# Kernel optimization log

Measured on AMD Instinct MI355X. Metric: run time of the kernel, lower is better.

Reference implementation:

```python
import jax, jax.numpy as jnp
import numpy as np

B, S, D, H = 4, 1024, 1024, 16
DK = D // H  # 64; concat head dim is 2*DK


def setup_inputs() -> dict:
    key = jax.random.key(0)
    ks = jax.random.split(key, 32)
    inp = {}
    for i, name in enumerate(["query_g", "key_g", "query_a", "key_a", "value_a"]):
        inp[name] = jax.random.normal(ks[i], (B, S, D), dtype=jnp.float32)
    inp["mask"] = jnp.ones((B, S, S), dtype=jnp.int32)
    w_scale = 1.0 / np.sqrt(D).astype(np.float32)
    # torch Linear weights are [out, in]; y = x @ W.T + b
    param_shapes = [
        ("Wqg", (D, D)), ("bqg", (D,)), ("Wkg", (D, D)), ("bkg", (D,)),
        ("Wqa", (D, D)), ("bqa", (D,)), ("Wka", (D, D)), ("bka", (D,)),
        ("Wva", (D, D)), ("bva", (D,)),
        ("Wgate", (D, 2 * D)), ("bgate", (D,)),
        ("Winfo", (D, D)), ("binfo", (D,)),
    ]
    for j, (name, shape) in enumerate(param_shapes):
        inp[name] = jax.random.normal(ks[5 + j], shape, dtype=jnp.float32) * w_scale
    return inp


def reference(query_g, key_g, query_a, key_a, value_a, mask,
              Wqg, bqg, Wkg, bkg, Wqa, bqa, Wka, bka, Wva, bva,
              Wgate, bgate, Winfo, binfo):
    def heads(x, W, b):
        # [B,S,D] -> [B,H,S,DK]
        return (x @ W.T + b).reshape(B, S, H, DK).transpose(0, 2, 1, 3)

    qg = heads(query_g, Wqg, bqg)
    kg = heads(key_g, Wkg, bkg)
    qa = heads(query_a, Wqa, bqa)
    ka = heads(key_a, Wka, bka)
    va = heads(value_a, Wva, bva)

    q = jnp.concatenate([qa, qg], axis=-1)  # [B,H,S,2*DK]
    k = jnp.concatenate([ka, kg], axis=-1)
    scores = jnp.einsum('bhqd,bhkd->bhqk', q, k) / np.float32(np.sqrt(2 * DK))
    scores = jnp.where(mask[:, None, :, :] == 0, jnp.float32(-1e9), scores)
    p_attn = jax.nn.softmax(scores, axis=-1)  # dropout is identity in eval
    x = jnp.einsum('bhqk,bhkd->bhqd', p_attn, va)
    x = x.transpose(0, 2, 1, 3).reshape(B, S, D)

    # GLU branch (dropout_glu is identity in eval); linears_out is identity
    gate = jax.nn.sigmoid(jnp.concatenate([query_a, query_g], axis=-1) @ Wgate.T + bgate)
    info = x @ Winfo.T + binfo
    return gate * info
```

## Files before the change

kernel.cpp:

```cpp
#include <hip/hip_runtime.h>


typedef unsigned short u16;
typedef __bf16 bf16x8 __attribute__((ext_vector_type(8)));
typedef float f32x4 __attribute__((ext_vector_type(4)));

#define DEV static __device__ __forceinline__

DEV u16 f2bf(float x) {
  union { __bf16 h; u16 u; } c;
  c.h = (__bf16)x;
  return c.u;
}
DEV float bf2f(u16 h) { return __uint_as_float(((unsigned)h) << 16); }

DEV bf16x8 cvt8(float4 a, float4 b) {
  bf16x8 v;
  v[0] = (__bf16)a.x; v[1] = (__bf16)a.y; v[2] = (__bf16)a.z; v[3] = (__bf16)a.w;
  v[4] = (__bf16)b.x; v[5] = (__bf16)b.y; v[6] = (__bf16)b.z; v[7] = (__bf16)b.w;
  return v;
}

struct Args {
  const float* act[5];
  const float* W[7];
  const float* bias[7];
  u16 *q_buf, *k_buf, *va_t, *x_buf, *g_buf;
  float* out;
};

__global__ __launch_bounds__(256, 2) void gemm_kernel(Args P, int unit_override) {
  __shared__ __align__(16) u16 As[128 * 40];
  __shared__ __align__(16) u16 Bs[128 * 40];

  int unit, bid;
  if (unit_override >= 0) { unit = unit_override; bid = blockIdx.x; }
  else { unit = blockIdx.x >> 8; bid = blockIdx.x & 255; }
  const int bm = bid & 31;
  const int bn = bid >> 5;

  const int tid = threadIdx.x;
  const int lane = tid & 63;
  const int wid = tid >> 6;
  const int wq = wid >> 1, wn = wid & 1;
  const int cl = lane & 15;
  const int gl = lane >> 4;

  const float *A0, *A1 = nullptr, *Wp, *bp;
  int nkt, mode;
  switch (unit) {
    case 0: A0 = P.act[0]; A1 = P.act[1]; Wp = P.W[5]; bp = P.bias[5]; nkt = 64; mode = 0; break;
    case 1: A0 = P.act[0]; Wp = P.W[0]; bp = P.bias[0]; nkt = 32; mode = 1; break;
    case 2: A0 = P.act[1]; Wp = P.W[1]; bp = P.bias[1]; nkt = 32; mode = 2; break;
    case 3: A0 = P.act[2]; Wp = P.W[2]; bp = P.bias[2]; nkt = 32; mode = 3; break;
    case 4: A0 = P.act[3]; Wp = P.W[3]; bp = P.bias[3]; nkt = 32; mode = 4; break;
    case 5: A0 = P.act[4]; Wp = P.W[4]; bp = P.bias[4]; nkt = 32; mode = 5; break;
    default: A0 = nullptr; Wp = P.W[6]; bp = P.bias[6]; nkt = 32; mode = 6; break;
  }
  const int K = nkt * 32;

  f32x4 acc[4][4];
  const f32x4 vzero = {0.f, 0.f, 0.f, 0.f};
#pragma unroll
  for (int i = 0; i < 4; i++)
#pragma unroll
    for (int j = 0; j < 4; j++) acc[i][j] = vzero;

  int arow[2], apn[2];
#pragma unroll
  for (int j = 0; j < 2; j++) {
    int f = (wid * 2 + j) * 64 + lane;
    arow[j] = f >> 2;
    apn[j] = f & 3;
  }

  float4 ra[2][2], rb[2][2];
  bf16x8 ra6[2];

  auto stage = [&](int kt) {
    const float* Abase;
    int akoff;
    if (A1 && kt >= 32) { Abase = A1; akoff = (kt - 32) * 32; }
    else { Abase = A0; akoff = kt * 32; }
#pragma unroll
    for (int j = 0; j < 2; j++) {
      size_t ae = (size_t)(bm * 128 + arow[j]) * 1024 + akoff + apn[j] * 8;
      size_t we = (size_t)(bn * 128 + arow[j]) * K + kt * 32 + apn[j] * 8;
      if (mode == 6) {
        ra6[j] = *(const bf16x8*)(const void*)(P.x_buf + ae);
      } else {
        const float* p = Abase + ae;
        ra[j][0] = *(const float4*)(const void*)p;
        ra[j][1] = *(const float4*)(const void*)(p + 4);
      }
      const float* q = Wp + we;
      rb[j][0] = *(const float4*)(const void*)q;
      rb[j][1] = *(const float4*)(const void*)(q + 4);
    }
  };

  stage(0);

  for (int kt = 0; kt < nkt; kt++) {
    __syncthreads();
#pragma unroll
    for (int j = 0; j < 2; j++) {
      *(bf16x8*)(void*)&As[arow[j] * 40 + apn[j] * 8] =
          (mode == 6) ? ra6[j] : cvt8(ra[j][0], ra[j][1]);
      *(bf16x8*)(void*)&Bs[arow[j] * 40 + apn[j] * 8] = cvt8(rb[j][0], rb[j][1]);
    }
    __syncthreads();

    bf16x8 af[4], bfr[4];
#pragma unroll
    for (int mi = 0; mi < 4; mi++)
      af[mi] = *(const bf16x8*)(const void*)&As[(wq * 64 + mi * 16 + cl) * 40 + gl * 8];
#pragma unroll
    for (int nj = 0; nj < 4; nj++)
      bfr[nj] = *(const bf16x8*)(const void*)&Bs[(wn * 64 + nj * 16 + cl) * 40 + gl * 8];

    if (kt + 1 < nkt) stage(kt + 1);

#pragma unroll
    for (int mi = 0; mi < 4; mi++)
#pragma unroll
      for (int nj = 0; nj < 4; nj++)
        acc[mi][nj] = __builtin_amdgcn_mfma_f32_16x16x32_bf16(af[mi], bfr[nj], acc[mi][nj], 0, 0, 0);
  }

  const int rowbase = bm * 128 + wq * 64;
  const int colbase = bn * 128 + wn * 64;
#pragma unroll
  for (int mi = 0; mi < 4; mi++) {
#pragma unroll
    for (int nj = 0; nj < 4; nj++) {
      const int gn = colbase + nj * 16 + cl;
      const float bias = bp[gn];
      const int gm0 = rowbase + mi * 16 + gl * 4;
      if (mode == 0) {
#pragma unroll
        for (int r = 0; r < 4; r++) {
          float v = acc[mi][nj][r] + bias;
          float s = 1.0f / (1.0f + __expf(-v));
          size_t idx = (size_t)(gm0 + r) * 1024 + gn;
          if (P.g_buf) P.g_buf[idx] = f2bf(s);
          else P.out[idx] = s;
        }
      } else if (mode <= 4) {
        u16* dst = (mode <= 2) ? P.q_buf : P.k_buf;
        const int part = (mode == 2 || mode == 4) ? 1 : 0;
        const int h = gn >> 6, dk = gn & 63;
#pragma unroll
        for (int r = 0; r < 4; r++) {
          int gm = gm0 + r;
          int b = gm >> 10, s = gm & 1023;
          dst[(((size_t)(b * 16 + h)) * 1024 + s) * 128 + part * 64 + dk] =
              f2bf(acc[mi][nj][r] + bias);
        }
      } else if (mode == 5) {
        const int h = gn >> 6, dk = gn & 63;
        int b = gm0 >> 10, s = gm0 & 1023;
        ushort4 pk;
        pk.x = f2bf(acc[mi][nj][0] + bias);
        pk.y = f2bf(acc[mi][nj][1] + bias);
        pk.z = f2bf(acc[mi][nj][2] + bias);
        pk.w = f2bf(acc[mi][nj][3] + bias);
        *(ushort4*)&P.va_t[(((size_t)(b * 16 + h)) * 64 + dk) * 1024 + s] = pk;
      } else {
#pragma unroll
        for (int r = 0; r < 4; r++) {
          size_t idx = (size_t)(gm0 + r) * 1024 + gn;
          float g = P.g_buf ? bf2f(P.g_buf[idx]) : P.out[idx];
          P.out[idx] = (acc[mi][nj][r] + bias) * g;
        }
      }
    }
  }
}

__global__ __launch_bounds__(256, 2) void attn_kernel(const u16* __restrict__ q_buf,
                                                      const u16* __restrict__ k_buf,
                                                      const u16* __restrict__ va_t,
                                                      const int* __restrict__ mask,
                                                      u16* __restrict__ x_buf) {
  __shared__ __align__(16) u16 Ks[64 * 136];
  __shared__ __align__(16) u16 Vs[64 * 72];
  __shared__ __align__(16) u16 Ps[4 * 32 * 72];
  __shared__ int mflags[16];

  const int tid = threadIdx.x;
  const int lane = tid & 63;
  const int wid = tid >> 6;
  const int cl = lane & 15;
  const int gl = lane >> 4;

  const int qt = blockIdx.x & 7;
  const int bh = blockIdx.x >> 3;
  const int b = bh >> 4, h = bh & 15;
  const u16* qh = q_buf + (size_t)bh * 1024 * 128;
  const u16* kh = k_buf + (size_t)bh * 1024 * 128;
  const u16* vh = va_t + (size_t)bh * 64 * 1024;
  const int s0 = qt * 128;

  if (tid < 16) mflags[tid] = 1;
  __syncthreads();
  {
    const int* mbase = mask + ((size_t)b * 1024 + s0) * 1024 + tid * 4;
    int ok = 1;
#pragma unroll 4
    for (int i = 0; i < 128; i++) {
      const int4 m4 = *(const int4*)(const void*)(mbase + (size_t)i * 1024);
      if (!(m4.x && m4.y && m4.z && m4.w)) ok = 0;
    }
    if (!ok) atomicAnd(&mflags[tid >> 4], 0);
  }
  __syncthreads();

  bf16x8 aq[2][4];
#pragma unroll
  for (int mi = 0; mi < 2; mi++) {
    int row = s0 + wid * 32 + mi * 16 + cl;
#pragma unroll
    for (int kk = 0; kk < 4; kk++)
      aq[mi][kk] = *(const bf16x8*)(const void*)&qh[(size_t)row * 128 + kk * 32 + gl * 8];
  }

  f32x4 acc_o[2][4];
  float l_part[2][4];
  const f32x4 vzero = {0.f, 0.f, 0.f, 0.f};
#pragma unroll
  for (int mi = 0; mi < 2; mi++) {
#pragma unroll
    for (int nj = 0; nj < 4; nj++) acc_o[mi][nj] = vzero;
#pragma unroll
    for (int r = 0; r < 4; r++) l_part[mi][r] = 0.f;
  }

  const float scale = 0.08838834764831845f;
  u16* pw = &Ps[wid * 32 * 72];

  int krow[4], kp[4], vrow[2], vp[2];
#pragma unroll
  for (int j = 0; j < 4; j++) {
    int f = (wid * 4 + j) * 64 + lane;
    krow[j] = f >> 4; kp[j] = f & 15;
  }
#pragma unroll
  for (int j = 0; j < 2; j++) {
    int f = (wid * 2 + j) * 64 + lane;
    vrow[j] = f >> 3; vp[j] = f & 7;
  }

  bf16x8 kv[4], vv[2];
  auto stageKV = [&](int kt) {
#pragma unroll
    for (int j = 0; j < 4; j++)
      kv[j] = *(const bf16x8*)(const void*)&kh[(size_t)(kt * 64 + krow[j]) * 128 + kp[j] * 8];
#pragma unroll
    for (int j = 0; j < 2; j++)
      vv[j] = *(const bf16x8*)(const void*)&vh[(size_t)vrow[j] * 1024 + kt * 64 + vp[j] * 8];
  };

  stageKV(0);

  for (int kt = 0; kt < 16; kt++) {
    __syncthreads();
#pragma unroll
    for (int j = 0; j < 4; j++)
      *(bf16x8*)(void*)&Ks[krow[j] * 136 + kp[j] * 8] = kv[j];
#pragma unroll
    for (int j = 0; j < 2; j++)
      *(bf16x8*)(void*)&Vs[vrow[j] * 72 + vp[j] * 8] = vv[j];
    __syncthreads();

    if (kt < 15) stageKV(kt + 1);

    f32x4 sc[2][4];
#pragma unroll
    for (int mi = 0; mi < 2; mi++)
#pragma unroll
      for (int nj = 0; nj < 4; nj++) sc[mi][nj] = vzero;
#pragma unroll
    for (int kk = 0; kk < 4; kk++) {
      bf16x8 bk[4];
#pragma unroll
      for (int nj = 0; nj < 4; nj++)
        bk[nj] = *(const bf16x8*)(const void*)&Ks[(nj * 16 + cl) * 136 + (kk * 4 + gl) * 8];
#pragma unroll
      for (int mi = 0; mi < 2; mi++)
#pragma unroll
        for (int nj = 0; nj < 4; nj++)
          sc[mi][nj] = __builtin_amdgcn_mfma_f32_16x16x32_bf16(aq[mi][kk], bk[nj], sc[mi][nj], 0, 0, 0);
    }

    const bool fastm = (mflags[kt] != 0);
#pragma unroll
    for (int mi = 0; mi < 2; mi++) {
#pragma unroll
      for (int nj = 0; nj < 4; nj++) {
        int key = kt * 64 + nj * 16 + cl;
#pragma unroll
        for (int r = 0; r < 4; r++) {
          int lrow = mi * 16 + gl * 4 + r;
          float sv = fminf(sc[mi][nj][r] * scale, 30.0f);
          float pv;
          if (fastm) {
            pv = __expf(sv);
          } else {
            int qrow = s0 + wid * 32 + lrow;
            int mv = mask[((size_t)b * 1024 + qrow) * 1024 + key];
            pv = (mv != 0) ? __expf(sv) : 0.0f;
          }
          l_part[mi][r] += pv;
          pw[lrow * 72 + nj * 16 + cl] = f2bf(pv);
        }
      }
    }

#pragma unroll
    for (int kk = 0; kk < 2; kk++) {
      bf16x8 ap[2], bv[4];
#pragma unroll
      for (int mi = 0; mi < 2; mi++)
        ap[mi] = *(const bf16x8*)(const void*)&pw[(mi * 16 + cl) * 72 + kk * 32 + gl * 8];
#pragma unroll
      for (int nj = 0; nj < 4; nj++)
        bv[nj] = *(const bf16x8*)(const void*)&Vs[(nj * 16 + cl) * 72 + (kk * 4 + gl) * 8];
#pragma unroll
      for (int mi = 0; mi < 2; mi++)
#pragma unroll
        for (int nj = 0; nj < 4; nj++)
          acc_o[mi][nj] = __builtin_amdgcn_mfma_f32_16x16x32_bf16(ap[mi], bv[nj], acc_o[mi][nj], 0, 0, 0);
    }
  }

#pragma unroll
  for (int mi = 0; mi < 2; mi++)
#pragma unroll
    for (int r = 0; r < 4; r++) {
      float s = l_part[mi][r];
      s += __shfl_xor(s, 1);
      s += __shfl_xor(s, 2);
      s += __shfl_xor(s, 4);
      s += __shfl_xor(s, 8);
      l_part[mi][r] = 1.0f / s;
    }

#pragma unroll
  for (int mi = 0; mi < 2; mi++)
#pragma unroll
    for (int nj = 0; nj < 4; nj++)
#pragma unroll
      for (int r = 0; r < 4; r++) {
        int srow = s0 + wid * 32 + mi * 16 + gl * 4 + r;
        int dv = nj * 16 + cl;
        float v = acc_o[mi][nj][r] * l_part[mi][r];
        x_buf[((size_t)b * 1024 + srow) * 1024 + h * 64 + dv] = f2bf(v);
      }
}

extern "C" void kernel_launch(void* const* d_in, const int* in_sizes, int n_in,
                              void* d_out, int out_size, void* d_ws, size_t ws_size,
                              hipStream_t stream) {
  (void)in_sizes; (void)n_in; (void)out_size;
  const int* mask = (const int*)d_in[5];

  char* ws = (char*)d_ws;
  u16* q_buf = (u16*)(ws);
  u16* k_buf = (u16*)(ws + ((size_t)16 << 20));
  u16* va_t  = (u16*)(ws + ((size_t)32 << 20));
  u16* x_buf = (u16*)(ws + ((size_t)40 << 20));
  u16* g_buf = (ws_size >= ((size_t)56 << 20)) ? (u16*)(ws + ((size_t)48 << 20)) : nullptr;

  Args P;
  P.act[0] = (const float*)d_in[2];
  P.act[1] = (const float*)d_in[0];
  P.act[2] = (const float*)d_in[3];
  P.act[3] = (const float*)d_in[1];
  P.act[4] = (const float*)d_in[4];
  P.W[0] = (const float*)d_in[10];  P.bias[0] = (const float*)d_in[11];
  P.W[1] = (const float*)d_in[6];   P.bias[1] = (const float*)d_in[7];
  P.W[2] = (const float*)d_in[12];  P.bias[2] = (const float*)d_in[13];
  P.W[3] = (const float*)d_in[8];   P.bias[3] = (const float*)d_in[9];
  P.W[4] = (const float*)d_in[14];  P.bias[4] = (const float*)d_in[15];
  P.W[5] = (const float*)d_in[16];  P.bias[5] = (const float*)d_in[17];
  P.W[6] = (const float*)d_in[18];  P.bias[6] = (const float*)d_in[19];
  P.q_buf = q_buf; P.k_buf = k_buf; P.va_t = va_t; P.x_buf = x_buf;
  P.g_buf = g_buf; P.out = (float*)d_out;

  hipLaunchKernelGGL(gemm_kernel, dim3(1536), dim3(256), 0, stream, P, -1);
  hipLaunchKernelGGL(attn_kernel, dim3(512), dim3(256), 0, stream,
                     q_buf, k_buf, va_t, mask, x_buf);
  hipLaunchKernelGGL(gemm_kernel, dim3(256), dim3(256), 0, stream, P, 6);
}
```

Before: 430.0 us.

## Pre-convert inputs to bf16 and use double-buffered global-to-LDS DMA GEMM

Adds a conversion kernel that casts all activations and weights from fp32 to bf16 into workspace once per call. A new GEMM kernel then streams bf16 tiles straight into LDS with global_load_lds, double-buffered, at higher occupancy. The aim is to halve the bytes the GEMMs read and to drop the per-tile in-register conversion and LDS store work. In exchange it adds an extra memory-bound pass plus a launch, and it only runs when the workspace is at least 112 MB; otherwise the old path is kept.

Measured after the change: 370.2 us. 13.9% less time.

```diff
diff --git a/kernel.cpp b/kernel.cpp
--- a/kernel.cpp
+++ b/kernel.cpp
@@ -19,6 +19,178 @@
   v[0] = (__bf16)a.x; v[1] = (__bf16)a.y; v[2] = (__bf16)a.z; v[3] = (__bf16)a.w;
   v[4] = (__bf16)b.x; v[5] = (__bf16)b.y; v[6] = (__bf16)b.z; v[7] = (__bf16)b.w;
   return v;
+}
+
+DEV void gload_lds16(const void* g, void* l) {
+  __builtin_amdgcn_global_load_lds(
+      (const __attribute__((address_space(1))) void*)g,
+      (__attribute__((address_space(3))) void*)l, 16, 0, 0);
+}
+
+struct CvtArgs {
+  const float* src[12];
+  u16* dst[12];
+  int n8[12];
+};
+
+__global__ __launch_bounds__(256) void cvt_kernel(CvtArgs C) {
+  const int stride = gridDim.x * blockDim.x;
+#pragma unroll 1
+  for (int s = 0; s < 12; ++s) {
+    const float4* src = (const float4*)C.src[s];
+    u16* dst = C.dst[s];
+    const int n8 = C.n8[s];
+    for (int i = blockIdx.x * blockDim.x + threadIdx.x; i < n8; i += stride) {
+      const float4 a = src[i * 2];
+      const float4 b = src[i * 2 + 1];
+      *(bf16x8*)(void*)(dst + (size_t)i * 8) = cvt8(a, b);
+    }
+  }
+}
+
+struct ArgsD {
+  const u16* act[5];
+  const u16* W[7];
+  const float* bias[7];
+  u16 *q_buf, *k_buf, *va_t, *x_buf, *g_buf;
+  float* out;
+};
+
+__global__ __launch_bounds__(256, 4) void gemm_dma(ArgsD P, int unit_override) {
+  __shared__ __align__(16) u16 As[2][128 * 32];
+  __shared__ __align__(16) u16 Bs[2][128 * 32];
+
+  int unit, bid;
+  if (unit_override >= 0) { unit = unit_override; bid = blockIdx.x; }
+  else { unit = blockIdx.x >> 8; bid = blockIdx.x & 255; }
+  const int bm = bid & 31;
+  const int bn = bid >> 5;
+
+  const int tid = threadIdx.x;
+  const int lane = tid & 63;
+  const int wid = tid >> 6;
+  const int wq = wid >> 1, wn = wid & 1;
+  const int cl = lane & 15;
+  const int gl = lane >> 4;
+
+  const u16 *A0, *A1 = nullptr, *Wp;
+  const float* bp;
+  int nkt, mode;
+  switch (unit) {
+    case 0: A0 = P.act[0]; A1 = P.act[1]; Wp = P.W[5]; bp = P.bias[5]; nkt = 64; mode = 0; break;
+    case 1: A0 = P.act[0]; Wp = P.W[0]; bp = P.bias[0]; nkt = 32; mode = 1; break;
+    case 2: A0 = P.act[1]; Wp = P.W[1]; bp = P.bias[1]; nkt = 32; mode = 2; break;
+    case 3: A0 = P.act[2]; Wp = P.W[2]; bp = P.bias[2]; nkt = 32; mode = 3; break;
+    case 4: A0 = P.act[3]; Wp = P.W[3]; bp = P.bias[3]; nkt = 32; mode = 4; break;
+    case 5: A0 = P.act[4]; Wp = P.W[4]; bp = P.bias[4]; nkt = 32; mode = 5; break;
+    default: A0 = P.x_buf; Wp = P.W[6]; bp = P.bias[6]; nkt = 32; mode = 6; break;
+  }
+  const int K = nkt * 32;
+
+  f32x4 acc[4][4];
+  const f32x4 vzero = {0.f, 0.f, 0.f, 0.f};
+#pragma unroll
+  for (int i = 0; i < 4; i++)
+#pragma unroll
+    for (int j = 0; j < 4; j++) acc[i][j] = vzero;
+
+  int drow[2];
+  const int dcol = (lane & 3) * 8;
+  drow[0] = (wid * 2 + 0) * 16 + (lane >> 2);
+  drow[1] = (wid * 2 + 1) * 16 + (lane >> 2);
+
+  auto STAGE = [&](int kt, int buf) {
+    const u16* Ab;
+    int akoff;
+    if (A1 && kt >= 32) { Ab = A1; akoff = (kt - 32) * 32; }
+    else { Ab = A0; akoff = kt * 32; }
+#pragma unroll
+    for (int i = 0; i < 2; ++i) {
+      gload_lds16(Ab + (size_t)(bm * 128 + drow[i]) * 1024 + akoff + dcol,
+                  &As[buf][(wid * 2 + i) * 512]);
+      gload_lds16(Wp + (size_t)(bn * 128 + drow[i]) * K + kt * 32 + dcol,
+                  &Bs[buf][(wid * 2 + i) * 512]);
+    }
+  };
+
+  STAGE(0, 0);
+
+  for (int kt = 0; kt < nkt; ++kt) {
+    const int cur = kt & 1;
+    __builtin_amdgcn_sched_barrier(0);
+    __builtin_amdgcn_s_barrier();
+    if (kt + 1 < nkt) {
+      STAGE(kt + 1, cur ^ 1);
+      asm volatile("s_waitcnt vmcnt(4)" ::: "memory");
+    } else {
+      asm volatile("s_waitcnt vmcnt(0)" ::: "memory");
+    }
+    __builtin_amdgcn_s_barrier();
+    __builtin_amdgcn_sched_barrier(0);
+
+    bf16x8 af[4], bfr[4];
+#pragma unroll
+    for (int mi = 0; mi < 4; mi++)
+      af[mi] = *(const bf16x8*)(const void*)&As[cur][(wq * 64 + mi * 16 + cl) * 32 + gl * 8];
+#pragma unroll
+    for (int nj = 0; nj < 4; nj++)
+      bfr[nj] = *(const bf16x8*)(const void*)&Bs[cur][(wn * 64 + nj * 16 + cl) * 32 + gl * 8];
+
+#pragma unroll
+    for (int mi = 0; mi < 4; mi++)
+#pragma unroll
+      for (int nj = 0; nj < 4; nj++)
+        acc[mi][nj] = __builtin_amdgcn_mfma_f32_16x16x32_bf16(af[mi], bfr[nj], acc[mi][nj], 0, 0, 0);
+  }
+
+  const int rowbase = bm * 128 + wq * 64;
+  const int colbase = bn * 128 + wn * 64;
+#pragma unroll
+  for (int mi = 0; mi < 4; mi++) {
+#pragma unroll
+    for (int nj = 0; nj < 4; nj++) {
+      const int gn = colbase + nj * 16 + cl;
+      const float bias = bp[gn];
+      const int gm0 = rowbase + mi * 16 + gl * 4;
+      if (mode == 0) {
+#pragma unroll
+        for (int r = 0; r < 4; r++) {
+          float v = acc[mi][nj][r] + bias;
+          float s = 1.0f / (1.0f + __expf(-v));
+          size_t idx = (size_t)(gm0 + r) * 1024 + gn;
+          if (P.g_buf) P.g_buf[idx] = f2bf(s);
+          else P.out[idx] = s;
+        }
+      } else if (mode <= 4) {
+        u16* dst = (mode <= 2) ? P.q_buf : P.k_buf;
+        const int part = (mode == 2 || mode == 4) ? 1 : 0;
+        const int h = gn >> 6, dk = gn & 63;
+#pragma unroll
+        for (int r = 0; r < 4; r++) {
+          int gm = gm0 + r;
+          int b = gm >> 10, s = gm & 1023;
+          dst[(((size_t)(b * 16 + h)) * 1024 + s) * 128 + part * 64 + dk] =
+              f2bf(acc[mi][nj][r] + bias);
+        }
+      } else if (mode == 5) {
+        const int h = gn >> 6, dk = gn & 63;
+        int b = gm0 >> 10, s = gm0 & 1023;
+        ushort4 pk;
+        pk.x = f2bf(acc[mi][nj][0] + bias);
+        pk.y = f2bf(acc[mi][nj][1] + bias);
+        pk.z = f2bf(acc[mi][nj][2] + bias);
+        pk.w = f2bf(acc[mi][nj][3] + bias);
+        *(ushort4*)&P.va_t[(((size_t)(b * 16 + h)) * 64 + dk) * 1024 + s] = pk;
+      } else {
+#pragma unroll
+        for (int r = 0; r < 4; r++) {
+          size_t idx = (size_t)(gm0 + r) * 1024 + gn;
+          float g = P.g_buf ? bf2f(P.g_buf[idx]) : P.out[idx];
+          P.out[idx] = (acc[mi][nj][r] + bias) * g;
+        }
+      }
+    }
+  }
 }
 
 struct Args {
@@ -372,24 +544,53 @@
   u16* x_buf = (u16*)(ws + ((size_t)40 << 20));
   u16* g_buf = (ws_size >= ((size_t)56 << 20)) ? (u16*)(ws + ((size_t)48 << 20)) : nullptr;
 
-  Args P;
-  P.act[0] = (const float*)d_in[2];
-  P.act[1] = (const float*)d_in[0];
-  P.act[2] = (const float*)d_in[3];
-  P.act[3] = (const float*)d_in[1];
-  P.act[4] = (const float*)d_in[4];
-  P.W[0] = (const float*)d_in[10];  P.bias[0] = (const float*)d_in[11];
-  P.W[1] = (const float*)d_in[6];   P.bias[1] = (const float*)d_in[7];
-  P.W[2] = (const float*)d_in[12];  P.bias[2] = (const float*)d_in[13];
-  P.W[3] = (const float*)d_in[8];   P.bias[3] = (const float*)d_in[9];
-  P.W[4] = (const float*)d_in[14];  P.bias[4] = (const float*)d_in[15];
-  P.W[5] = (const float*)d_in[16];  P.bias[5] = (const float*)d_in[17];
-  P.W[6] = (const float*)d_in[18];  P.bias[6] = (const float*)d_in[19];
-  P.q_buf = q_buf; P.k_buf = k_buf; P.va_t = va_t; P.x_buf = x_buf;
-  P.g_buf = g_buf; P.out = (float*)d_out;
-
-  hipLaunchKernelGGL(gemm_kernel, dim3(1536), dim3(256), 0, stream, P, -1);
-  hipLaunchKernelGGL(attn_kernel, dim3(512), dim3(256), 0, stream,
-                     q_buf, k_buf, va_t, mask, x_buf);
-  hipLaunchKernelGGL(gemm_kernel, dim3(256), dim3(256), 0, stream, P, 6);
-}
+  const int act_idx[5] = {2, 0, 3, 1, 4};
+  const int w_idx[7] = {10, 6, 12, 8, 14, 16, 18};
+  const int b_idx[7] = {11, 7, 13, 9, 15, 17, 19};
+
+  const bool big = (ws_size >= ((size_t)112 << 20)) && (g_buf != nullptr);
+
+  if (big) {
+    u16* actb[5];
+    for (int i = 0; i < 5; i++) actb[i] = (u16*)(ws + ((size_t)56 << 20) + (size_t)i * (8 << 20));
+    u16* wb[7];
+    for (int i = 0; i < 5; i++) wb[i] = (u16*)(ws + ((size_t)96 << 20) + (size_t)i * (2 << 20));
+    wb[5] = (u16*)(ws + ((size_t)106 << 20));
+    wb[6] = (u16*)(ws + ((size_t)110 << 20));
+
+    CvtArgs C;
+    for (int i = 0; i < 5; i++) {
+      C.src[i] = (const float*)d_in[act_idx[i]];
+      C.dst[i] = actb[i];
+      C.n8[i] = (4096 * 1024) / 8;
+    }
+    for (int i = 0; i < 7; i++) {
+      C.src[5 + i] = (const float*)d_in[w_idx[i]];
+      C.dst[5 + i] = wb[i];
+      C.n8[5 + i] = ((i == 5) ? (1024 * 2048) : (1024 * 1024)) / 8;
+    }
+    hipLaunchKernelGGL(cvt_kernel, dim3(2048), dim3(256), 0, stream, C);
+
+    ArgsD P;
+    for (int i = 0; i < 5; i++) P.act[i] = actb[i];
+    for (int i = 0; i < 7; i++) { P.W[i] = wb[i]; P.bias[i] = (const float*)d_in[b_idx[i]]; }
+    P.q_buf = q_buf; P.k_buf = k_buf; P.va_t = va_t; P.x_buf = x_buf;
+    P.g_buf = g_buf; P.out = (float*)d_out;
+
+    hipLaunchKernelGGL(gemm_dma, dim3(1536), dim3(256), 0, stream, P, -1);
+    hipLaunchKernelGGL(attn_kernel, dim3(512), dim3(256), 0, stream,
+                       q_buf, k_buf, va_t, mask, x_buf);
+    hipLaunchKernelGGL(gemm_dma, dim3(256), dim3(256), 0, stream, P, 6);
+  } else {
+    Args P;
+    for (int i = 0; i < 5; i++) P.act[i] = (const float*)d_in[act_idx[i]];
+    for (int i = 0; i < 7; i++) { P.W[i] = (const float*)d_in[w_idx[i]]; P.bias[i] = (const float*)d_in[b_idx[i]]; }
+    P.q_buf = q_buf; P.k_buf = k_buf; P.va_t = va_t; P.x_buf = x_buf;
+    P.g_buf = g_buf; P.out = (float*)d_out;
+
+    hipLaunchKernelGGL(gemm_kernel, dim3(1536), dim3(256), 0, stream, P, -1);
+    hipLaunchKernelGGL(attn_kernel, dim3(512), dim3(256), 0, stream,
+                       q_buf, k_buf, va_t, mask, x_buf);
+    hipLaunchKernelGGL(gemm_kernel, dim3(256), dim3(256), 0, stream, P, 6);
+  }
+}
```
